# Kernel tuning notes

Hardware: AMD Instinct MI355X
Metric: run time of the kernel (lower is better)

## Reference

```python
import jax, jax.numpy as jnp
import numpy as np
from jax import lax

B, C, H, W = 32, 128, 56, 56
SIZE = C * H * W
EPS = 1e-5
SLOPE = 0.1


def setup_inputs() -> dict:
    key = jax.random.key(0)
    ks = jax.random.split(key, 12)
    return {
        "ax": jax.random.normal(ks[0], (B, C, H, W), dtype=jnp.float32),
        "mx": jax.random.normal(ks[1], (B, C, H, W), dtype=jnp.float32),
        # grouped conv1d (groups=SIZE, k=2, no bias) == per-position pair weights [SIZE, 2]
        "cfc_w": jax.random.normal(ks[2], (SIZE, 2), dtype=jnp.float32) * 0.1,
        # BatchNorm1d (eval mode) params over SIZE channels
        "bn_gamma": jax.random.normal(ks[3], (SIZE,), dtype=jnp.float32) * 0.1 + 1.0,
        "bn_beta": jax.random.normal(ks[4], (SIZE,), dtype=jnp.float32) * 0.1,
        "bn_mean": jax.random.normal(ks[5], (SIZE,), dtype=jnp.float32) * 0.1,
        "bn_var": jax.random.uniform(ks[6], (SIZE,), dtype=jnp.float32, minval=0.5, maxval=1.5),
        # conv3x3, C->C, bias
        "conv_w": jax.random.normal(ks[7], (C, C, 3, 3), dtype=jnp.float32) * (1.0 / np.sqrt(C * 9)),
        "conv_b": jax.random.normal(ks[8], (C,), dtype=jnp.float32) * 0.01,
        # BatchNorm2d (eval mode) params over C channels
        "bn2_gamma": jax.random.normal(ks[9], (C,), dtype=jnp.float32) * 0.1 + 1.0,
        "bn2_beta": jax.random.normal(ks[10], (C,), dtype=jnp.float32) * 0.1,
        "bn2_mean": jax.random.normal(ks[11], (C,), dtype=jnp.float32) * 0.1,
        "bn2_var": jax.random.uniform(jax.random.fold_in(key, 99), (C,), dtype=jnp.float32, minval=0.5, maxval=1.5),
    }


def reference(ax, mx, cfc_w, bn_gamma, bn_beta, bn_mean, bn_var,
              conv_w, conv_b, bn2_gamma, bn2_beta, bn2_mean, bn2_var):
    b, c, h, w = ax.shape
    a = ax.reshape(b, -1)  # [B, SIZE]
    m = mx.reshape(b, -1)
    # degenerate grouped Conv1d(k=2, groups=SIZE): z_i = w_i0 * a_i + w_i1 * m_i
    z = cfc_w[:, 0] * a + cfc_w[:, 1] * m
    # BatchNorm1d (eval) + LeakyReLU(0.1)
    z = (z - bn_mean) * (bn_gamma / jnp.sqrt(bn_var + EPS)) + bn_beta
    z = jax.nn.leaky_relu(z, SLOPE).reshape(b, c, h, w)
    # conv3x3 (stride 1, pad 1) + bias
    y = lax.conv_general_dilated(z, conv_w, window_strides=(1, 1),
                                 padding=((1, 1), (1, 1)),
                                 dimension_numbers=("NCHW", "OIHW", "NCHW"))
    y = y + conv_b[None, :, None, None]
    # BatchNorm2d (eval) + LeakyReLU(0.1)
    scale = (bn2_gamma / jnp.sqrt(bn2_var + EPS))[None, :, None, None]
    y = (y - bn2_mean[None, :, None, None]) * scale + bn2_beta[None, :, None, None]
    return jax.nn.leaky_relu(y, SLOPE)
```

## Files before the change

### kernel.cpp

```cpp
#include <hip/hip_runtime.h>

#define B_ 32
#define C_ 128
#define H_ 56
#define W_ 56
#define HW_ (H_*W_)
#define SIZE_ (C_*HW_)
#define NPIX_ (B_*HW_)
#define HP_ 58
#define WP_ 58
#define PLSZ_ (B_*HP_*WP_*32)
#define K_ 1152
#define EPS_ 1e-5f
#define SLOPE_ 0.1f

typedef __bf16 bf16x8 __attribute__((ext_vector_type(8)));
typedef float  f32x4  __attribute__((ext_vector_type(4)));

__device__ __forceinline__ ushort f2bf(float x) {
    union { float f; unsigned u; } v; v.f = x;
    return (ushort)((v.u + 0x7FFFu + ((v.u >> 16) & 1u)) >> 16);
}
__device__ __forceinline__ float lrelu(float z) { return z > 0.f ? z : SLOPE_ * z; }

__device__ __forceinline__ void glds16(const ushort* g, ushort* l) {
    __builtin_amdgcn_global_load_lds(
        (const __attribute__((address_space(1))) unsigned int*)g,
        (__attribute__((address_space(3))) unsigned int*)l, 16, 0, 0);
}

__global__ __launch_bounds__(256) void prep_kernel(
    const float* __restrict__ conv_w, const float* __restrict__ conv_b,
    const float* __restrict__ g2, const float* __restrict__ b2,
    const float* __restrict__ m2, const float* __restrict__ v2,
    const float2* __restrict__ cfc, const float* __restrict__ g1,
    const float* __restrict__ b1, const float* __restrict__ mu1,
    const float* __restrict__ v1,
    ushort* __restrict__ wA, float* __restrict__ scale2, float* __restrict__ shift2,
    float* __restrict__ p0, float* __restrict__ p1, float* __restrict__ p2)
{
    int tid = blockIdx.x * 256 + threadIdx.x;
    if (tid < C_ * K_) {
        int co = tid / K_;
        int k  = tid - co * K_;
        int t  = k >> 5, kk = k & 31;
        int khkw = k >> 7, ci = k & 127;
        int kh = khkw / 3, kw = khkw - 3 * kh;
        wA[(t * C_ + co) * 32 + kk] = f2bf(conv_w[((co * C_ + ci) * 3 + kh) * 3 + kw]);
    }
    if (tid < C_) {
        float sc = g2[tid] * rsqrtf(v2[tid] + EPS_);
        scale2[tid] = sc;
        shift2[tid] = (conv_b[tid] - m2[tid]) * sc + b2[tid];
    }
    if (tid < SIZE_) {
        float sc = g1[tid] * rsqrtf(v1[tid] + EPS_);
        float2 wv = cfc[tid];
        p0[tid] = wv.x * sc;
        p1[tid] = wv.y * sc;
        p2[tid] = b1[tid] - mu1[tid] * sc;
    }
}

__global__ __launch_bounds__(256) void zfuse_kernel(
    const float4* __restrict__ ax, const float4* __restrict__ mx,
    const float4* __restrict__ p0, const float4* __restrict__ p1,
    const float4* __restrict__ p2, ushort* __restrict__ zp)
{
    __shared__ ushort tile[W_ * 132];
    const int hp = blockIdx.x, b = blockIdx.y;
    const int tid = threadIdx.x;
    const int rb = (b * HP_ + hp) * (WP_ * 32);
    if (hp == 0 || hp == HP_ - 1) {
        for (int ks = 0; ks < 4; ++ks) {
            uint2* r2 = (uint2*)(zp + ks * PLSZ_ + rb);
            for (int i = tid; i < WP_ * 32 / 4; i += 256) r2[i] = make_uint2(0u, 0u);
        }
        return;
    }
    const int h = hp - 1;
    const int base4 = (b * SIZE_) >> 2;
    for (int i = tid; i < 1792; i += 256) {
        int c  = i / 14;
        int w4 = i - c * 14;
        int s4 = c * (HW_ / 4) + h * (W_ / 4) + w4;
        float4 a = ax[base4 + s4];
        float4 m = mx[base4 + s4];
        float4 q0 = p0[s4], q1 = p1[s4], q2 = p2[s4];
        int wb = w4 * 4;
        tile[(wb + 0) * 132 + c] = f2bf(lrelu(a.x * q0.x + m.x * q1.x + q2.x));
        tile[(wb + 1) * 132 + c] = f2bf(lrelu(a.y * q0.y + m.y * q1.y + q2.y));
        tile[(wb + 2) * 132 + c] = f2bf(lrelu(a.z * q0.z + m.z * q1.z + q2.z));
        tile[(wb + 3) * 132 + c] = f2bf(lrelu(a.w * q0.w + m.w * q1.w + q2.w));
    }
    __syncthreads();
    {
        int side = (tid >> 7) & 1, ks = (tid >> 5) & 3, cc = tid & 31;
        zp[ks * PLSZ_ + rb + (side ? (WP_ - 1) * 32 : 0) + cc] = 0;
    }
    for (int j = tid; j < 1792; j += 256) {
        int ks = j / 448, r = j - ks * 448;
        int w = r >> 3, cc = r & 7;
        *(uint2*)(zp + ks * PLSZ_ + rb + (w + 1) * 32 + cc * 4) =
            *(const uint2*)(tile + w * 132 + ks * 32 + cc * 4);
    }
}

__global__ __launch_bounds__(256, 3) void conv_kernel(
    const ushort* __restrict__ zp, const ushort* __restrict__ wA,
    const float* __restrict__ scale2, const float* __restrict__ shift2,
    float* __restrict__ out)
{
    __shared__ ushort As[3][128 * 32];
    __shared__ ushort Bs[3][128 * 32];

    const int tid  = threadIdx.x;
    const int wave = tid >> 6, lane = tid & 63;
    const int l16  = lane & 15, quad = lane >> 4;
    const int bid  = blockIdx.x;
    const int pbase = ((bid & 7) * 98 + (bid >> 3)) * 128;

    const int srow = wave * 32 + (lane >> 2);
    const int skey = (srow >> 1) & 3;
    const int sch  = (lane & 3) ^ skey;
    const ushort* agA = wA + srow * 32 + sch * 8;

    int pf0 = pbase + srow;
    int bb0 = pf0 / HW_, pi0 = pf0 - bb0 * HW_;
    int h0 = pi0 / W_, w0 = pi0 - h0 * W_;
    const ushort* bgB0 = zp + ((bb0 * HP_ + h0) * WP_ + w0) * 32 + sch * 8;
    int pf1 = pf0 + 16;
    int bb1 = pf1 / HW_, pi1 = pf1 - bb1 * HW_;
    int h1 = pi1 / W_, w1 = pi1 - h1 * W_;
    const ushort* bgB1 = zp + ((bb1 * HP_ + h1) * WP_ + w1) * 32 + sch * 8;

    const int lofs0 = (wave * 32) * 32;
    const int lofs1 = (wave * 32 + 16) * 32;

    const int cob = (wave & 1) * 64;
    const int pxb = (wave >> 1) * 64;
    const int rquad = quad ^ ((l16 >> 1) & 3);

    f32x4 acc[4][4] = {};

#define STAGE(buf, t)                                                      \
    do {                                                                   \
        glds16(agA + (t) * 4096,        As[buf] + lofs0);                  \
        glds16(agA + (t) * 4096 + 512,  As[buf] + lofs1);                  \
        glds16(bgB0 + BOFF(t),          Bs[buf] + lofs0);                  \
        glds16(bgB1 + BOFF(t),          Bs[buf] + lofs1);                  \
    } while (0)

#define BOFF(t) (((t) & 3) * PLSZ_ + (((((t) >> 2) / 3) * WP_ + (((t) >> 2) % 3)) * 32))

    STAGE(0, 0);
    STAGE(1, 1);

    #pragma unroll
    for (int t = 0; t < 36; ++t) {
        if (t < 35) asm volatile("s_waitcnt vmcnt(4)" ::: "memory");
        else        asm volatile("s_waitcnt vmcnt(0)" ::: "memory");
        __builtin_amdgcn_s_barrier();
        __builtin_amdgcn_sched_barrier(0);
        if (t <= 33) {
            STAGE((t + 2) % 3, t + 2);
        }
        const int buf = t % 3;
        bf16x8 af[4], bfr[4];
        #pragma unroll
        for (int mt = 0; mt < 4; ++mt)
            af[mt] = *(const bf16x8*)(As[buf] + (cob + mt * 16 + l16) * 32 + rquad * 8);
        #pragma unroll
        for (int nt = 0; nt < 4; ++nt)
            bfr[nt] = *(const bf16x8*)(Bs[buf] + (pxb + nt * 16 + l16) * 32 + rquad * 8);
        #pragma unroll
        for (int mt = 0; mt < 4; ++mt)
            #pragma unroll
            for (int nt = 0; nt < 4; ++nt)
                acc[mt][nt] = __builtin_amdgcn_mfma_f32_16x16x32_bf16(
                    af[mt], bfr[nt], acc[mt][nt], 0, 0, 0);
    }
#undef STAGE
#undef BOFF

    int pob[4];
    #pragma unroll
    for (int nt = 0; nt < 4; ++nt) {
        int pf = pbase + pxb + nt * 16 + l16;
        int bb = pf / HW_;
        pob[nt] = bb * SIZE_ + (pf - bb * HW_);
    }
    #pragma unroll
    for (int mt = 0; mt < 4; ++mt) {
        #pragma unroll
        for (int r = 0; r < 4; ++r) {
            int co = cob + mt * 16 + quad * 4 + r;
            float sc = scale2[co], sh = shift2[co];
            #pragma unroll
            for (int nt = 0; nt < 4; ++nt) {
                float v = acc[mt][nt][r] * sc + sh;
                out[(size_t)pob[nt] + co * HW_] = lrelu(v);
            }
        }
    }
}

extern "C" void kernel_launch(void* const* d_in, const int* in_sizes, int n_in,
                              void* d_out, int out_size, void* d_ws, size_t ws_size,
                              hipStream_t stream) {
    const float* ax     = (const float*)d_in[0];
    const float* mx     = (const float*)d_in[1];
    const float* cfc    = (const float*)d_in[2];
    const float* bn_g   = (const float*)d_in[3];
    const float* bn_b   = (const float*)d_in[4];
    const float* bn_m   = (const float*)d_in[5];
    const float* bn_v   = (const float*)d_in[6];
    const float* conv_w = (const float*)d_in[7];
    const float* conv_b = (const float*)d_in[8];
    const float* g2     = (const float*)d_in[9];
    const float* b2     = (const float*)d_in[10];
    const float* m2     = (const float*)d_in[11];
    const float* v2     = (const float*)d_in[12];
    float* out = (float*)d_out;

    char* ws = (char*)d_ws;
    ushort* zp     = (ushort*)ws;
    ushort* wA     = (ushort*)(ws + 27557888);
    float*  scale2 = (float*)(ws + 27852800);
    float*  shift2 = (float*)(ws + 27853312);
    float*  p0     = (float*)(ws + 27853824);
    float*  p1     = (float*)(ws + 29459456);
    float*  p2     = (float*)(ws + 31065088);

    prep_kernel<<<dim3((SIZE_ + 255) / 256), 256, 0, stream>>>(
        conv_w, conv_b, g2, b2, m2, v2, (const float2*)cfc,
        bn_g, bn_b, bn_m, bn_v, wA, scale2, shift2, p0, p1, p2);
    zfuse_kernel<<<dim3(HP_, B_), 256, 0, stream>>>(
        (const float4*)ax, (const float4*)mx,
        (const float4*)p0, (const float4*)p1, (const float4*)p2, zp);
    conv_kernel<<<dim3(NPIX_ / 128), 256, 0, stream>>>(zp, wA, scale2, shift2, out);
}
```

Baseline: 237.2 us.

## Enlarge conv tile to 256 pixels with 512 threads and K-step 64

```diff
diff --git a/kernel.cpp b/kernel.cpp
--- a/kernel.cpp
+++ b/kernel.cpp
@@ -43,10 +43,10 @@
     if (tid < C_ * K_) {
         int co = tid / K_;
         int k  = tid - co * K_;
-        int t  = k >> 5, kk = k & 31;
         int khkw = k >> 7, ci = k & 127;
         int kh = khkw / 3, kw = khkw - 3 * kh;
-        wA[(t * C_ + co) * 32 + kk] = f2bf(conv_w[((co * C_ + ci) * 3 + kh) * 3 + kw]);
+        wA[((k >> 6) * C_ + co) * 64 + (k & 63)] =
+            f2bf(conv_w[((co * C_ + ci) * 3 + kh) * 3 + kw]);
     }
     if (tid < C_) {
         float sc = g2[tid] * rsqrtf(v2[tid] + EPS_);
@@ -106,82 +106,93 @@
     }
 }
 
-__global__ __launch_bounds__(256, 3) void conv_kernel(
+__global__ __launch_bounds__(512, 2) void conv_kernel(
     const ushort* __restrict__ zp, const ushort* __restrict__ wA,
     const float* __restrict__ scale2, const float* __restrict__ shift2,
     float* __restrict__ out)
 {
-    __shared__ ushort As[3][128 * 32];
-    __shared__ ushort Bs[3][128 * 32];
+    __shared__ ushort As[3][128 * 64];
+    __shared__ ushort Bs[3][256 * 64];
 
     const int tid  = threadIdx.x;
     const int wave = tid >> 6, lane = tid & 63;
     const int l16  = lane & 15, quad = lane >> 4;
     const int bid  = blockIdx.x;
-    const int pbase = ((bid & 7) * 98 + (bid >> 3)) * 128;
-
-    const int srow = wave * 32 + (lane >> 2);
-    const int skey = (srow >> 1) & 3;
-    const int sch  = (lane & 3) ^ skey;
-    const ushort* agA = wA + srow * 32 + sch * 8;
-
-    int pf0 = pbase + srow;
-    int bb0 = pf0 / HW_, pi0 = pf0 - bb0 * HW_;
-    int h0 = pi0 / W_, w0 = pi0 - h0 * W_;
-    const ushort* bgB0 = zp + ((bb0 * HP_ + h0) * WP_ + w0) * 32 + sch * 8;
-    int pf1 = pf0 + 16;
-    int bb1 = pf1 / HW_, pi1 = pf1 - bb1 * HW_;
-    int h1 = pi1 / W_, w1 = pi1 - h1 * W_;
-    const ushort* bgB1 = zp + ((bb1 * HP_ + h1) * WP_ + w1) * 32 + sch * 8;
-
-    const int lofs0 = (wave * 32) * 32;
-    const int lofs1 = (wave * 32 + 16) * 32;
+    const int pbase = ((bid & 7) * 49 + (bid >> 3)) * 256;
+
+    const int c_swz = (lane & 7) ^ ((lane >> 3) & 7);
+    const ushort* agA = wA + (16 * wave + (lane >> 3)) * 64 + c_swz * 8;
+
+    const ushort* bgB[4];
+    #pragma unroll
+    for (int j = 0; j < 4; ++j) {
+        int pxl = 32 * wave + 8 * j + (lane >> 3);
+        int pf  = pbase + pxl;
+        int bb  = pf / HW_, pi = pf - bb * HW_;
+        int h   = pi / W_, w = pi - h * W_;
+        bgB[j] = zp + (c_swz >> 2) * PLSZ_
+                    + ((bb * HP_ + h) * WP_ + w) * 32 + (c_swz & 3) * 8;
+    }
 
     const int cob = (wave & 1) * 64;
     const int pxb = (wave >> 1) * 64;
-    const int rquad = quad ^ ((l16 >> 1) & 3);
+    const int ch0 = ((quad ^ (l16 & 7))) * 8;
+    const int ch1 = ch0 ^ 32;
 
     f32x4 acc[4][4] = {};
 
-#define STAGE(buf, t)                                                      \
-    do {                                                                   \
-        glds16(agA + (t) * 4096,        As[buf] + lofs0);                  \
-        glds16(agA + (t) * 4096 + 512,  As[buf] + lofs1);                  \
-        glds16(bgB0 + BOFF(t),          Bs[buf] + lofs0);                  \
-        glds16(bgB1 + BOFF(t),          Bs[buf] + lofs1);                  \
+#define BDEL(t) (((t) & 1) * 2 * PLSZ_ + \
+                 (((((t) >> 1) / 3) * WP_ + (((t) >> 1) % 3)) * 32))
+
+#define STAGE(t, buf) do {                                              \
+        glds16(agA + (t) * 8192,        &As[buf][wave * 1024]);         \
+        glds16(agA + (t) * 8192 + 512,  &As[buf][wave * 1024 + 512]);   \
+        glds16(bgB[0] + BDEL(t), &Bs[buf][wave * 2048]);                \
+        glds16(bgB[1] + BDEL(t), &Bs[buf][wave * 2048 + 512]);          \
+        glds16(bgB[2] + BDEL(t), &Bs[buf][wave * 2048 + 1024]);         \
+        glds16(bgB[3] + BDEL(t), &Bs[buf][wave * 2048 + 1536]);         \
     } while (0)
-
-#define BOFF(t) (((t) & 3) * PLSZ_ + (((((t) >> 2) / 3) * WP_ + (((t) >> 2) % 3)) * 32))
 
     STAGE(0, 0);
     STAGE(1, 1);
 
     #pragma unroll
-    for (int t = 0; t < 36; ++t) {
-        if (t < 35) asm volatile("s_waitcnt vmcnt(4)" ::: "memory");
+    for (int t = 0; t < 18; ++t) {
+        __builtin_amdgcn_sched_barrier(0);
+        if (t < 17) asm volatile("s_waitcnt vmcnt(6)" ::: "memory");
         else        asm volatile("s_waitcnt vmcnt(0)" ::: "memory");
         __builtin_amdgcn_s_barrier();
         __builtin_amdgcn_sched_barrier(0);
-        if (t <= 33) {
-            STAGE((t + 2) % 3, t + 2);
-        }
+        if (t <= 15) STAGE(t + 2, (t + 2) % 3);
+
         const int buf = t % 3;
-        bf16x8 af[4], bfr[4];
-        #pragma unroll
-        for (int mt = 0; mt < 4; ++mt)
-            af[mt] = *(const bf16x8*)(As[buf] + (cob + mt * 16 + l16) * 32 + rquad * 8);
-        #pragma unroll
-        for (int nt = 0; nt < 4; ++nt)
-            bfr[nt] = *(const bf16x8*)(Bs[buf] + (pxb + nt * 16 + l16) * 32 + rquad * 8);
+        bf16x8 af0[4], af1[4], bf0[4], bf1[4];
+        #pragma unroll
+        for (int mt = 0; mt < 4; ++mt) {
+            const ushort* ar = &As[buf][(cob + mt * 16 + l16) * 64];
+            af0[mt] = *(const bf16x8*)(ar + ch0);
+            af1[mt] = *(const bf16x8*)(ar + ch1);
+        }
+        #pragma unroll
+        for (int nt = 0; nt < 4; ++nt) {
+            const ushort* br = &Bs[buf][(pxb + nt * 16 + l16) * 64];
+            bf0[nt] = *(const bf16x8*)(br + ch0);
+            bf1[nt] = *(const bf16x8*)(br + ch1);
+        }
+        __builtin_amdgcn_s_setprio(1);
         #pragma unroll
         for (int mt = 0; mt < 4; ++mt)
             #pragma unroll
-            for (int nt = 0; nt < 4; ++nt)
+            for (int nt = 0; nt < 4; ++nt) {
                 acc[mt][nt] = __builtin_amdgcn_mfma_f32_16x16x32_bf16(
-                    af[mt], bfr[nt], acc[mt][nt], 0, 0, 0);
+                    af0[mt], bf0[nt], acc[mt][nt], 0, 0, 0);
+                acc[mt][nt] = __builtin_amdgcn_mfma_f32_16x16x32_bf16(
+                    af1[mt], bf1[nt], acc[mt][nt], 0, 0, 0);
+            }
+        __builtin_amdgcn_s_setprio(0);
     }
 #undef STAGE
-#undef BOFF
+#undef BDEL
 
     int pob[4];
     #pragma unroll
@@ -238,5 +249,5 @@
     zfuse_kernel<<<dim3(HP_, B_), 256, 0, stream>>>(
         (const float4*)ax, (const float4*)mx,
         (const float4*)p0, (const float4*)p1, (const float4*)p2, zp);
-    conv_kernel<<<dim3(NPIX_ / 128), 256, 0, stream>>>(zp, wA, scale2, shift2, out);
-}
+    conv_kernel<<<dim3(NPIX_ / 256), 512, 0, stream>>>(zp, wA, scale2, shift2, out);
+}
```

Result: faster. 230.7 us (-2.8%).
